# Performance work log

Measured on AMD Instinct MI355X. Metric: run time of the kernel, lower is better.

Reference implementation:

```python
import jax, jax.numpy as jnp
import numpy as np

NUM_HEADS = 8
HEAD_DIM = 16
NEG_SLOPE = 0.2


def setup_inputs() -> dict:
    key = jax.random.key(0)
    k1, k2, k3, k4, k5 = jax.random.split(key, 5)
    N, E, D_IN, D_OUT = 100000, 1600000, 128, 128
    x = jax.random.normal(k1, (N, D_IN), dtype=jnp.float32)
    edge_indices = jax.random.randint(k2, (2, E), 0, N, dtype=jnp.int64)
    W = jax.random.normal(k3, (D_OUT, D_IN), dtype=jnp.float32) * (1.0 / np.sqrt(D_IN))
    src_attn = jax.random.normal(k4, (1, NUM_HEADS, HEAD_DIM), dtype=jnp.float32) * (1.0 / np.sqrt(HEAD_DIM))
    dst_attn = jax.random.normal(k5, (1, NUM_HEADS, HEAD_DIM), dtype=jnp.float32) * (1.0 / np.sqrt(HEAD_DIM))
    return {"x": x, "edge_indices": edge_indices, "W": W, "src_attn": src_attn, "dst_attn": dst_attn}


def reference(x, edge_indices, W, src_attn, dst_attn):
    N = x.shape[0]
    # add self loops (i, i) for every node
    loops = jnp.arange(N, dtype=edge_indices.dtype)
    ei = jnp.concatenate([edge_indices, jnp.stack([loops, loops])], axis=1)  # [2, E+N]
    row, col = ei[0], ei[1]

    # linear projection + head split: [N, H, hd]
    h = (x @ W.T).reshape(N, NUM_HEADS, HEAD_DIM)

    # per-node attention logits, gathered per edge: [E', H]
    s = jnp.sum(h * src_attn, axis=-1)  # [N, H]
    d = jnp.sum(h * dst_attn, axis=-1)  # [N, H]
    e = jax.nn.leaky_relu(s[row] + d[col], negative_slope=NEG_SLOPE)  # [E', H]

    # sparse softmax over each row's neighborhood (dim=1 of the sparse matrix)
    m = jax.ops.segment_max(e, row, num_segments=N)  # [N, H]
    e = jnp.exp(e - m[row])
    z = jax.ops.segment_sum(e, row, num_segments=N)  # [N, H]
    a = e / z[row]  # [E', H]

    # per-head SpMM: out[row] += a * h[col]
    out = jax.ops.segment_sum(a[:, :, None] * h[col], row, num_segments=N)  # [N, H, hd]
    return out.reshape(N, NUM_HEADS * HEAD_DIM)
```

## Files before the change

kernel.cpp:

```cpp
#include <hip/hip_runtime.h>
#include <hip/hip_bf16.h>
#include <math.h>

#define NEG_SLOPE 0.2f

typedef __attribute__((ext_vector_type(8))) short short8v;
typedef __attribute__((ext_vector_type(4))) float f32x4;

__global__ __launch_bounds__(256) void gat_prep(
    const float* __restrict__ W, const float* __restrict__ srcA,
    const float* __restrict__ dstA, ushort* __restrict__ wbf)
{
  int tid = blockIdx.x * 256 + threadIdx.x;
  if (tid >= 36 * 64) return;
  int frag = tid >> 6, lane = tid & 63;
  int nt = frag >> 2, ks = frag & 3;
  int kbase = ks * 32 + (lane >> 4) * 8;
  ushort v[8];
  if (nt < 8) {
    int r = nt * 16 + (lane & 15);
#pragma unroll
    for (int j = 0; j < 8; ++j)
      v[j] = __bfloat16_as_ushort(__float2bfloat16(W[(size_t)r * 128 + kbase + j]));
  } else {
    int n = lane & 15;
    int hd = n & 7;
    const float* av = (n < 8) ? srcA : dstA;
#pragma unroll
    for (int j = 0; j < 8; ++j) {
      float acc = 0.f;
      int k = kbase + j;
      for (int d = 0; d < 16; ++d)
        acc += W[(size_t)(hd * 16 + d) * 128 + k] * av[hd * 16 + d];
      v[j] = __bfloat16_as_ushort(__float2bfloat16(acc));
    }
  }
  ushort* dst = wbf + ((size_t)frag * 64 + lane) * 8;
#pragma unroll
  for (int j = 0; j < 8; ++j) dst[j] = v[j];
}

__global__ __launch_bounds__(256, 2) void gat_gemm_mfma(
    const float* __restrict__ x, const ushort* __restrict__ wbf,
    ushort* __restrict__ hb, float* __restrict__ s, float* __restrict__ dv,
    int N, int nchunks)
{
  const int wave = threadIdx.x >> 6, lane = threadIdx.x & 63;
  const int lrow = lane & 15, lkg = lane >> 4;

  short8v b[36];
  const short8v* wv = (const short8v*)wbf;
#pragma unroll
  for (int f = 0; f < 36; ++f) b[f] = wv[(size_t)f * 64 + lane];

  for (int chunk = blockIdx.x; chunk < nchunks; chunk += gridDim.x) {
    const int r0 = chunk * 64 + wave * 16;
    int arow = r0 + lrow; if (arow > N - 1) arow = N - 1;
    const float* xr = x + (size_t)arow * 128 + lkg * 8;

    f32x4 acc[9];
#pragma unroll
    for (int t = 0; t < 9; ++t) acc[t] = (f32x4){0.f, 0.f, 0.f, 0.f};

#pragma unroll
    for (int ks = 0; ks < 4; ++ks) {
      float4 x0 = *(const float4*)(xr + ks * 32);
      float4 x1 = *(const float4*)(xr + ks * 32 + 4);
      short8v a;
      a[0] = (short)__bfloat16_as_ushort(__float2bfloat16(x0.x));
      a[1] = (short)__bfloat16_as_ushort(__float2bfloat16(x0.y));
      a[2] = (short)__bfloat16_as_ushort(__float2bfloat16(x0.z));
      a[3] = (short)__bfloat16_as_ushort(__float2bfloat16(x0.w));
      a[4] = (short)__bfloat16_as_ushort(__float2bfloat16(x1.x));
      a[5] = (short)__bfloat16_as_ushort(__float2bfloat16(x1.y));
      a[6] = (short)__bfloat16_as_ushort(__float2bfloat16(x1.z));
      a[7] = (short)__bfloat16_as_ushort(__float2bfloat16(x1.w));
#pragma unroll
      for (int t = 0; t < 9; ++t)
        acc[t] = __builtin_amdgcn_mfma_f32_16x16x32_bf16(a, b[t * 4 + ks], acc[t], 0, 0, 0);
    }

    const int rbase = r0 + lkg * 4;
#pragma unroll
    for (int t = 0; t < 8; ++t) {
#pragma unroll
      for (int r = 0; r < 4; ++r) {
        int row = rbase + r;
        if (row < N)
          hb[(size_t)row * 128 + t * 16 + lrow] =
              __bfloat16_as_ushort(__float2bfloat16(acc[t][r]));
      }
    }
#pragma unroll
    for (int r = 0; r < 4; ++r) {
      int row = rbase + r;
      if (row < N) {
        if (lrow < 8) s[(size_t)row * 8 + lrow] = acc[8][r];
        else          dv[(size_t)row * 8 + (lrow - 8)] = acc[8][r];
      }
    }
  }
}

__global__ void gat_detect(const int* __restrict__ ei, int E, int* __restrict__ flag)
{
  __shared__ int any;
  if (threadIdx.x == 0) any = 0;
  __syncthreads();
  int n = E < 512 ? E : 512;
  int local = 0;
  for (int i = threadIdx.x; i < n; i += 256)
    if (ei[2 * i + 1] != 0) local = 1;
  if (local) atomicOr(&any, 1);
  __syncthreads();
  if (threadIdx.x == 0) *flag = (any == 0) ? 1 : 0;
}

__global__ __launch_bounds__(256) void gat_hist(
    const int* __restrict__ ei, int E, const int* __restrict__ flag,
    int* __restrict__ count, int* __restrict__ rank, int userank)
{
  const int is64 = *flag;
  int i = blockIdx.x * 256 + threadIdx.x;
  const int stride = gridDim.x * 256;
  for (; i < E; i += stride) {
    int r = is64 ? ei[2 * i] : ei[i];
    int old = atomicAdd(&count[r], 1);
    if (userank) rank[i] = old;
  }
}

__global__ __launch_bounds__(256) void gat_scan_part(
    const int* __restrict__ count, int N, int* __restrict__ partial)
{
  __shared__ int sm[256];
  int base = blockIdx.x * 1024;
  int tsum = 0;
  for (int i = threadIdx.x; i < 1024; i += 256) {
    int idx = base + i;
    if (idx < N) tsum += count[idx] + 1;
  }
  sm[threadIdx.x] = tsum;
  __syncthreads();
  for (int off = 128; off > 0; off >>= 1) {
    if (threadIdx.x < off) sm[threadIdx.x] += sm[threadIdx.x + off];
    __syncthreads();
  }
  if (threadIdx.x == 0) partial[blockIdx.x] = sm[0];
}

__global__ __launch_bounds__(1024) void gat_scan_mid(int* __restrict__ partial, int nb)
{
  __shared__ int sm[1024];
  int t = threadIdx.x;
  int v = (t < nb) ? partial[t] : 0;
  sm[t] = v;
  __syncthreads();
  int acc = v;
  for (int off = 1; off < 1024; off <<= 1) {
    int other = (t >= off) ? sm[t - off] : 0;
    __syncthreads();
    acc += other;
    sm[t] = acc;
    __syncthreads();
  }
  if (t < nb) partial[t] = acc - v;
}

__global__ __launch_bounds__(256) void gat_scan_final(
    const int* __restrict__ count, int N, const int* __restrict__ partial,
    int* __restrict__ offsets, int* __restrict__ cursor, int total)
{
  __shared__ int sm[256];
  int base = blockIdx.x * 1024 + threadIdx.x * 4;
  int v[4];
  int tsum = 0;
#pragma unroll
  for (int j = 0; j < 4; ++j) {
    int idx = base + j;
    v[j] = (idx < N) ? (count[idx] + 1) : 0;
    tsum += v[j];
  }
  sm[threadIdx.x] = tsum;
  __syncthreads();
  int acc = tsum;
  for (int off = 1; off < 256; off <<= 1) {
    int other = (threadIdx.x >= off) ? sm[threadIdx.x - off] : 0;
    __syncthreads();
    acc += other;
    sm[threadIdx.x] = acc;
    __syncthreads();
  }
  int ex = acc - tsum + partial[blockIdx.x];
#pragma unroll
  for (int j = 0; j < 4; ++j) {
    int idx = base + j;
    if (idx < N) { offsets[idx] = ex; cursor[idx] = ex; ex += v[j]; }
  }
  if (blockIdx.x == 0 && threadIdx.x == 0) offsets[N] = total;
}

__global__ __launch_bounds__(256) void gat_scatter_rank(
    const int* __restrict__ ei, int E, int N, const int* __restrict__ flag,
    const int* __restrict__ offsets, const int* __restrict__ count,
    const int* __restrict__ rank, int* __restrict__ scol)
{
  const int is64 = *flag;
  int i = blockIdx.x * 256 + threadIdx.x;
  const int stride = gridDim.x * 256;
  const int total = E + N;
  for (; i < total; i += stride) {
    int pos, c;
    if (i < E) {
      int r;
      if (is64) { r = ei[2 * i]; c = ei[2 * (E + i)]; }
      else      { r = ei[i];     c = ei[E + i]; }
      pos = offsets[r] + rank[i];
    } else {
      int r = i - E; c = r;
      pos = offsets[r] + count[r];
    }
    scol[pos] = c;
  }
}

__global__ __launch_bounds__(256) void gat_scatter(
    const int* __restrict__ ei, int E, int N, const int* __restrict__ flag,
    int* __restrict__ cursor, int* __restrict__ scol)
{
  const int is64 = *flag;
  int i = blockIdx.x * 256 + threadIdx.x;
  const int stride = gridDim.x * 256;
  const int total = E + N;
  for (; i < total; i += stride) {
    int r, c;
    if (i < E) {
      if (is64) { r = ei[2 * i]; c = ei[2 * (E + i)]; }
      else      { r = ei[i];     c = ei[E + i]; }
    } else {
      r = i - E; c = r;
    }
    int pos = atomicAdd(&cursor[r], 1);
    scol[pos] = c;
  }
}

__global__ __launch_bounds__(256) void gat_agg(
    const uint* __restrict__ hb, const float* __restrict__ s, const float* __restrict__ dv,
    const int* __restrict__ offsets, const int* __restrict__ scol,
    float* __restrict__ out, int N)
{
  int wid = (int)((blockIdx.x * 256 + threadIdx.x) >> 6);
  int lane = threadIdx.x & 63;
  if (wid >= N) return;
  const int head = lane >> 3;
  const int beg = __builtin_amdgcn_readfirstlane(offsets[wid]);
  const int end = __builtin_amdgcn_readfirstlane(offsets[wid + 1]);
  const float sl = s[wid * 8 + head];

  const char* hbp = (const char*)hb;
  const char* dvp = (const char*)dv;
  const uint hoff = (uint)lane * 4u;
  const uint doff = (uint)head * 4u;

  int c1 = scol[beg];
  int i1 = (beg + 1 < end) ? (beg + 1) : (end - 1);
  int c2 = scol[i1];
  float dl0 = *(const float*)(dvp + ((uint)c1 * 32u + doff));
  uint  hu0 = *(const uint*)(hbp + ((uint)c1 * 256u + hoff));

  float z = 0.f, ax = 0.f, ay = 0.f;
  for (int i = beg; i < end; ++i) {
    int i2 = (i + 2 < end) ? (i + 2) : (end - 1);
    int c3 = scol[i2];
    float dl1 = *(const float*)(dvp + ((uint)c2 * 32u + doff));
    uint  hu1 = *(const uint*)(hbp + ((uint)c2 * 256u + hoff));

    float hx = __uint_as_float(hu0 << 16);
    float hy = __uint_as_float(hu0 & 0xFFFF0000u);
    float e = sl + dl0;
    e = fmaxf(e, NEG_SLOPE * e);
    float w = __expf(e);
    z += w;
    ax = fmaf(w, hx, ax);
    ay = fmaf(w, hy, ay);

    c2 = c3; dl0 = dl1; hu0 = hu1;
  }
  float inv = 1.f / z;
  *(float2*)(out + (size_t)wid * 128 + lane * 2) = make_float2(ax * inv, ay * inv);
}

extern "C" void kernel_launch(void* const* d_in, const int* in_sizes, int n_in,
                              void* d_out, int out_size, void* d_ws, size_t ws_size,
                              hipStream_t stream) {
  const float* x    = (const float*)d_in[0];
  const int*   ei   = (const int*)d_in[1];
  const float* W    = (const float*)d_in[2];
  const float* srcA = (const float*)d_in[3];
  const float* dstA = (const float*)d_in[4];
  float* out = (float*)d_out;
  const int N = in_sizes[0] / 128;
  const int E = in_sizes[1] / 2;

  ushort* hbuf = (ushort*)d_ws;
  float* s  = (float*)(hbuf + (size_t)N * 128);
  float* dv = s + (size_t)N * 8;
  ushort* wbf = (ushort*)(dv + (size_t)N * 8);
  int* count   = (int*)((char*)wbf + 36864);
  int* offsets = count + N;
  int* cursor  = offsets + (N + 1);
  int* partial = cursor + N;
  int* flag    = partial + 1024;
  int* scol    = flag + 4;
  int* rank    = scol + (E + N);

  const size_t need_rank = (size_t)((char*)(rank + E) - (char*)d_ws);
  const int userank = (ws_size >= need_rank) ? 1 : 0;

  const int nchunks = (N + 63) / 64;

  (void)hipMemsetAsync(count, 0, (size_t)N * sizeof(int), stream);
  gat_prep<<<9, 256, 0, stream>>>(W, srcA, dstA, wbf);
  gat_gemm_mfma<<<512, 256, 0, stream>>>(x, wbf, hbuf, s, dv, N, nchunks);
  gat_detect<<<1, 256, 0, stream>>>(ei, E, flag);
  gat_hist<<<2048, 256, 0, stream>>>(ei, E, flag, count, rank, userank);
  const int nb = (N + 1023) / 1024;
  gat_scan_part<<<nb, 256, 0, stream>>>(count, N, partial);
  gat_scan_mid<<<1, 1024, 0, stream>>>(partial, nb);
  gat_scan_final<<<nb, 256, 0, stream>>>(count, N, partial, offsets, cursor, E + N);
  if (userank)
    gat_scatter_rank<<<2048, 256, 0, stream>>>(ei, E, N, flag, offsets, count, rank, scol);
  else
    gat_scatter<<<2048, 256, 0, stream>>>(ei, E, N, flag, cursor, scol);
  gat_agg<<<(N + 3) / 4, 256, 0, stream>>>((const uint*)hbuf, s, dv, offsets, scol, out, N);
}
```

Baseline: 251.0 us.

## Fuse GEMM with edge histogram, inline int64 detection, widen aggregation gathers

The count memset moves into the prep kernel. The GEMM and the row histogram now run in one launch, with one block in five doing MFMA work and the other four doing atomics, so the compute-bound and atomic-bound phases can overlap. Each block now detects the 64-bit index format itself, which removes the separate detect kernel. The aggregation kernel splits each wave into four groups that process four edges at once, with 16-byte gathers per lane and a cross-group shuffle reduction. This trades more registers and shuffle work for fewer, wider memory requests.

```diff
diff --git a/kernel.cpp b/kernel.cpp
--- a/kernel.cpp
+++ b/kernel.cpp
@@ -9,8 +9,12 @@
 
 __global__ __launch_bounds__(256) void gat_prep(
     const float* __restrict__ W, const float* __restrict__ srcA,
-    const float* __restrict__ dstA, ushort* __restrict__ wbf)
-{
+    const float* __restrict__ dstA, ushort* __restrict__ wbf,
+    int* __restrict__ count, int N)
+{
+  for (int i = blockIdx.x * 256 + threadIdx.x; i < N; i += gridDim.x * 256)
+    count[i] = 0;
+
   int tid = blockIdx.x * 256 + threadIdx.x;
   if (tid >= 36 * 64) return;
   int frag = tid >> 6, lane = tid & 63;
@@ -40,93 +44,88 @@
   for (int j = 0; j < 8; ++j) dst[j] = v[j];
 }
 
-__global__ __launch_bounds__(256, 2) void gat_gemm_mfma(
+__global__ __launch_bounds__(256, 2) void gat_gemm_hist(
     const float* __restrict__ x, const ushort* __restrict__ wbf,
     ushort* __restrict__ hb, float* __restrict__ s, float* __restrict__ dv,
-    int N, int nchunks)
-{
-  const int wave = threadIdx.x >> 6, lane = threadIdx.x & 63;
-  const int lrow = lane & 15, lkg = lane >> 4;
-
-  short8v b[36];
-  const short8v* wv = (const short8v*)wbf;
-#pragma unroll
-  for (int f = 0; f < 36; ++f) b[f] = wv[(size_t)f * 64 + lane];
-
-  for (int chunk = blockIdx.x; chunk < nchunks; chunk += gridDim.x) {
-    const int r0 = chunk * 64 + wave * 16;
-    int arow = r0 + lrow; if (arow > N - 1) arow = N - 1;
-    const float* xr = x + (size_t)arow * 128 + lkg * 8;
-
-    f32x4 acc[9];
-#pragma unroll
-    for (int t = 0; t < 9; ++t) acc[t] = (f32x4){0.f, 0.f, 0.f, 0.f};
-
-#pragma unroll
-    for (int ks = 0; ks < 4; ++ks) {
-      float4 x0 = *(const float4*)(xr + ks * 32);
-      float4 x1 = *(const float4*)(xr + ks * 32 + 4);
-      short8v a;
-      a[0] = (short)__bfloat16_as_ushort(__float2bfloat16(x0.x));
-      a[1] = (short)__bfloat16_as_ushort(__float2bfloat16(x0.y));
-      a[2] = (short)__bfloat16_as_ushort(__float2bfloat16(x0.z));
-      a[3] = (short)__bfloat16_as_ushort(__float2bfloat16(x0.w));
-      a[4] = (short)__bfloat16_as_ushort(__float2bfloat16(x1.x));
-      a[5] = (short)__bfloat16_as_ushort(__float2bfloat16(x1.y));
-      a[6] = (short)__bfloat16_as_ushort(__float2bfloat16(x1.z));
-      a[7] = (short)__bfloat16_as_ushort(__float2bfloat16(x1.w));
-#pragma unroll
-      for (int t = 0; t < 9; ++t)
-        acc[t] = __builtin_amdgcn_mfma_f32_16x16x32_bf16(a, b[t * 4 + ks], acc[t], 0, 0, 0);
-    }
-
-    const int rbase = r0 + lkg * 4;
-#pragma unroll
-    for (int t = 0; t < 8; ++t) {
+    int N, int nchunks, int G1,
+    const int* __restrict__ ei, int E, int* __restrict__ count,
+    int* __restrict__ rank, int userank)
+{
+  const int q = (int)blockIdx.x / 5;
+  const int r5 = (int)blockIdx.x % 5;
+  if (r5 == 0) {
+    const int wave = threadIdx.x >> 6, lane = threadIdx.x & 63;
+    const int lrow = lane & 15, lkg = lane >> 4;
+
+    short8v b[36];
+    const short8v* wv = (const short8v*)wbf;
+#pragma unroll
+    for (int f = 0; f < 36; ++f) b[f] = wv[(size_t)f * 64 + lane];
+
+    for (int chunk = q; chunk < nchunks; chunk += G1) {
+      const int r0 = chunk * 64 + wave * 16;
+      int arow = r0 + lrow; if (arow > N - 1) arow = N - 1;
+      const float* xr = x + (size_t)arow * 128 + lkg * 8;
+
+      f32x4 acc[9];
+#pragma unroll
+      for (int t = 0; t < 9; ++t) acc[t] = (f32x4){0.f, 0.f, 0.f, 0.f};
+
+#pragma unroll
+      for (int ks = 0; ks < 4; ++ks) {
+        float4 x0 = *(const float4*)(xr + ks * 32);
+        float4 x1 = *(const float4*)(xr + ks * 32 + 4);
+        short8v a;
+        a[0] = (short)__bfloat16_as_ushort(__float2bfloat16(x0.x));
+        a[1] = (short)__bfloat16_as_ushort(__float2bfloat16(x0.y));
+        a[2] = (short)__bfloat16_as_ushort(__float2bfloat16(x0.z));
+        a[3] = (short)__bfloat16_as_ushort(__float2bfloat16(x0.w));
+        a[4] = (short)__bfloat16_as_ushort(__float2bfloat16(x1.x));
+        a[5] = (short)__bfloat16_as_ushort(__float2bfloat16(x1.y));
+        a[6] = (short)__bfloat16_as_ushort(__float2bfloat16(x1.z));
+        a[7] = (short)__bfloat16_as_ushort(__float2bfloat16(x1.w));
+#pragma unroll
+        for (int t = 0; t < 9; ++t)
+          acc[t] = __builtin_amdgcn_mfma_f32_16x16x32_bf16(a, b[t * 4 + ks], acc[t], 0, 0, 0);
+      }
+
+      const int rbase = r0 + lkg * 4;
+#pragma unroll
+      for (int t = 0; t < 8; ++t) {
+#pragma unroll
+        for (int r = 0; r < 4; ++r) {
+          int row = rbase + r;
+          if (row < N)
+            hb[(size_t)row * 128 + t * 16 + lrow] =
+                __bfloat16_as_ushort(__float2bfloat16(acc[t][r]));
+        }
+      }
 #pragma unroll
       for (int r = 0; r < 4; ++r) {
         int row = rbase + r;
-        if (row < N)
-          hb[(size_t)row * 128 + t * 16 + lrow] =
-              __bfloat16_as_ushort(__float2bfloat16(acc[t][r]));
+        if (row < N) {
+          if (lrow < 8) s[(size_t)row * 8 + lrow] = acc[8][r];
+          else          dv[(size_t)row * 8 + (lrow - 8)] = acc[8][r];
+        }
       }
     }
-#pragma unroll
-    for (int r = 0; r < 4; ++r) {
-      int row = rbase + r;
-      if (row < N) {
-        if (lrow < 8) s[(size_t)row * 8 + lrow] = acc[8][r];
-        else          dv[(size_t)row * 8 + (lrow - 8)] = acc[8][r];
-      }
-    }
-  }
-}
-
-__global__ void gat_detect(const int* __restrict__ ei, int E, int* __restrict__ flag)
-{
-  __shared__ int any;
-  if (threadIdx.x == 0) any = 0;
-  __syncthreads();
-  int n = E < 512 ? E : 512;
-  int local = 0;
-  for (int i = threadIdx.x; i < n; i += 256)
-    if (ei[2 * i + 1] != 0) local = 1;
-  if (local) atomicOr(&any, 1);
-  __syncthreads();
-  if (threadIdx.x == 0) *flag = (any == 0) ? 1 : 0;
-}
-
-__global__ __launch_bounds__(256) void gat_hist(
-    const int* __restrict__ ei, int E, const int* __restrict__ flag,
-    int* __restrict__ count, int* __restrict__ rank, int userank)
-{
-  const int is64 = *flag;
-  int i = blockIdx.x * 256 + threadIdx.x;
-  const int stride = gridDim.x * 256;
-  for (; i < E; i += stride) {
-    int r = is64 ? ei[2 * i] : ei[i];
-    int old = atomicAdd(&count[r], 1);
-    if (userank) rank[i] = old;
+  } else {
+    __shared__ int sh64;
+    if (threadIdx.x == 0) sh64 = 1;
+    __syncthreads();
+    if (ei[2 * threadIdx.x + 1] != 0) sh64 = 0;
+    __syncthreads();
+    const int is64 = sh64;
+
+    const int hb_id = q * 4 + (r5 - 1);
+    const int nhb = 4 * G1;
+    int i = hb_id * 256 + threadIdx.x;
+    const int stride = nhb * 256;
+    for (; i < E; i += stride) {
+      int r = is64 ? ei[2 * i] : ei[i];
+      int old = atomicAdd(&count[r], 1);
+      if (userank) rank[i] = old;
+    }
   }
 }
 
@@ -201,11 +200,17 @@
 }
 
 __global__ __launch_bounds__(256) void gat_scatter_rank(
-    const int* __restrict__ ei, int E, int N, const int* __restrict__ flag,
+    const int* __restrict__ ei, int E, int N,
     const int* __restrict__ offsets, const int* __restrict__ count,
     const int* __restrict__ rank, int* __restrict__ scol)
 {
-  const int is64 = *flag;
+  __shared__ int sh64;
+  if (threadIdx.x == 0) sh64 = 1;
+  __syncthreads();
+  if (ei[2 * threadIdx.x + 1] != 0) sh64 = 0;
+  __syncthreads();
+  const int is64 = sh64;
+
   int i = blockIdx.x * 256 + threadIdx.x;
   const int stride = gridDim.x * 256;
   const int total = E + N;
@@ -225,10 +230,16 @@
 }
 
 __global__ __launch_bounds__(256) void gat_scatter(
-    const int* __restrict__ ei, int E, int N, const int* __restrict__ flag,
+    const int* __restrict__ ei, int E, int N,
     int* __restrict__ cursor, int* __restrict__ scol)
 {
-  const int is64 = *flag;
+  __shared__ int sh64;
+  if (threadIdx.x == 0) sh64 = 1;
+  __syncthreads();
+  if (ei[2 * threadIdx.x + 1] != 0) sh64 = 0;
+  __syncthreads();
+  const int is64 = sh64;
+
   int i = blockIdx.x * 256 + threadIdx.x;
   const int stride = gridDim.x * 256;
   const int total = E + N;
@@ -253,42 +264,69 @@
   int wid = (int)((blockIdx.x * 256 + threadIdx.x) >> 6);
   int lane = threadIdx.x & 63;
   if (wid >= N) return;
-  const int head = lane >> 3;
+  const int g = lane >> 4;
+  const int t = lane & 15;
+  const int head = t >> 1;
   const int beg = __builtin_amdgcn_readfirstlane(offsets[wid]);
   const int end = __builtin_amdgcn_readfirstlane(offsets[wid + 1]);
   const float sl = s[wid * 8 + head];
 
   const char* hbp = (const char*)hb;
   const char* dvp = (const char*)dv;
-  const uint hoff = (uint)lane * 4u;
+  const uint hoff = (uint)t * 16u;
   const uint doff = (uint)head * 4u;
 
-  int c1 = scol[beg];
-  int i1 = (beg + 1 < end) ? (beg + 1) : (end - 1);
-  int c2 = scol[i1];
-  float dl0 = *(const float*)(dvp + ((uint)c1 * 32u + doff));
-  uint  hu0 = *(const uint*)(hbp + ((uint)c1 * 256u + hoff));
-
-  float z = 0.f, ax = 0.f, ay = 0.f;
-  for (int i = beg; i < end; ++i) {
-    int i2 = (i + 2 < end) ? (i + 2) : (end - 1);
-    int c3 = scol[i2];
-    float dl1 = *(const float*)(dvp + ((uint)c2 * 32u + doff));
-    uint  hu1 = *(const uint*)(hbp + ((uint)c2 * 256u + hoff));
-
-    float hx = __uint_as_float(hu0 << 16);
-    float hy = __uint_as_float(hu0 & 0xFFFF0000u);
-    float e = sl + dl0;
+  float z = 0.f;
+  float a0 = 0, a1 = 0, a2 = 0, a3 = 0, a4 = 0, a5 = 0, a6 = 0, a7 = 0;
+
+  const int nq = (end - beg + 3) >> 2;
+  const int lasti = end - 1;
+
+  int iA = beg + g;       iA = iA < end ? iA : lasti;
+  int iB = beg + 4 + g;   iB = iB < end ? iB : lasti;
+  int cA = scol[iA];
+  int cB = scol[iB];
+  float dlA = *(const float*)(dvp + ((uint)cA * 32u + doff));
+  uint4 huA = *(const uint4*)(hbp + ((uint)cA * 256u + hoff));
+
+  for (int j = 0; j < nq; ++j) {
+    int iC = beg + 4 * (j + 2) + g; iC = iC < end ? iC : lasti;
+    int cC = scol[iC];
+    float dlB = *(const float*)(dvp + ((uint)cB * 32u + doff));
+    uint4 huB = *(const uint4*)(hbp + ((uint)cB * 256u + hoff));
+
+    float e = sl + dlA;
     e = fmaxf(e, NEG_SLOPE * e);
-    float w = __expf(e);
+    float w = (beg + 4 * j + g < end) ? __expf(e) : 0.f;
     z += w;
-    ax = fmaf(w, hx, ax);
-    ay = fmaf(w, hy, ay);
-
-    c2 = c3; dl0 = dl1; hu0 = hu1;
-  }
+    a0 = fmaf(w, __uint_as_float(huA.x << 16), a0);
+    a1 = fmaf(w, __uint_as_float(huA.x & 0xFFFF0000u), a1);
+    a2 = fmaf(w, __uint_as_float(huA.y << 16), a2);
+    a3 = fmaf(w, __uint_as_float(huA.y & 0xFFFF0000u), a3);
+    a4 = fmaf(w, __uint_as_float(huA.z << 16), a4);
+    a5 = fmaf(w, __uint_as_float(huA.z & 0xFFFF0000u), a5);
+    a6 = fmaf(w, __uint_as_float(huA.w << 16), a6);
+    a7 = fmaf(w, __uint_as_float(huA.w & 0xFFFF0000u), a7);
+
+    cB = cC; dlA = dlB; huA = huB;
+  }
+
+  a0 += __shfl_xor(a0, 16, 64); a0 += __shfl_xor(a0, 32, 64);
+  a1 += __shfl_xor(a1, 16, 64); a1 += __shfl_xor(a1, 32, 64);
+  a2 += __shfl_xor(a2, 16, 64); a2 += __shfl_xor(a2, 32, 64);
+  a3 += __shfl_xor(a3, 16, 64); a3 += __shfl_xor(a3, 32, 64);
+  a4 += __shfl_xor(a4, 16, 64); a4 += __shfl_xor(a4, 32, 64);
+  a5 += __shfl_xor(a5, 16, 64); a5 += __shfl_xor(a5, 32, 64);
+  a6 += __shfl_xor(a6, 16, 64); a6 += __shfl_xor(a6, 32, 64);
+  a7 += __shfl_xor(a7, 16, 64); a7 += __shfl_xor(a7, 32, 64);
+  z  += __shfl_xor(z, 16, 64);  z  += __shfl_xor(z, 32, 64);
+
   float inv = 1.f / z;
-  *(float2*)(out + (size_t)wid * 128 + lane * 2) = make_float2(ax * inv, ay * inv);
+  if (lane < 16) {
+    float4* op = (float4*)(out + (size_t)wid * 128 + t * 8);
+    op[0] = make_float4(a0 * inv, a1 * inv, a2 * inv, a3 * inv);
+    op[1] = make_float4(a4 * inv, a5 * inv, a6 * inv, a7 * inv);
+  }
 }
 
 extern "C" void kernel_launch(void* const* d_in, const int* in_sizes, int n_in,
@@ -311,27 +349,25 @@
   int* offsets = count + N;
   int* cursor  = offsets + (N + 1);
   int* partial = cursor + N;
-  int* flag    = partial + 1024;
-  int* scol    = flag + 4;
+  int* scol    = partial + 1024;
   int* rank    = scol + (E + N);
 
   const size_t need_rank = (size_t)((char*)(rank + E) - (char*)d_ws);
   const int userank = (ws_size >= need_rank) ? 1 : 0;
 
   const int nchunks = (N + 63) / 64;
-
-  (void)hipMemsetAsync(count, 0, (size_t)N * sizeof(int), stream);
-  gat_prep<<<9, 256, 0, stream>>>(W, srcA, dstA, wbf);
-  gat_gemm_mfma<<<512, 256, 0, stream>>>(x, wbf, hbuf, s, dv, N, nchunks);
-  gat_detect<<<1, 256, 0, stream>>>(ei, E, flag);
-  gat_hist<<<2048, 256, 0, stream>>>(ei, E, flag, count, rank, userank);
+  const int G1 = 512;
+
+  gat_prep<<<2048, 256, 0, stream>>>(W, srcA, dstA, wbf, count, N);
+  gat_gemm_hist<<<5 * G1, 256, 0, stream>>>(x, wbf, hbuf, s, dv, N, nchunks, G1,
+                                            ei, E, count, rank, userank);
   const int nb = (N + 1023) / 1024;
   gat_scan_part<<<nb, 256, 0, stream>>>(count, N, partial);
   gat_scan_mid<<<1, 1024, 0, stream>>>(partial, nb);
   gat_scan_final<<<nb, 256, 0, stream>>>(count, N, partial, offsets, cursor, E + N);
   if (userank)
-    gat_scatter_rank<<<2048, 256, 0, stream>>>(ei, E, N, flag, offsets, count, rank, scol);
+    gat_scatter_rank<<<2048, 256, 0, stream>>>(ei, E, N, offsets, count, rank, scol);
   else
-    gat_scatter<<<2048, 256, 0, stream>>>(ei, E, N, flag, cursor, scol);
+    gat_scatter<<<2048, 256, 0, stream>>>(ei, E, N, cursor, scol);
   gat_agg<<<(N + 3) / 4, 256, 0, stream>>>((const uint*)hbuf, s, dv, offsets, scol, out, N);
 }
```

After: 202.9 us. 1.24x faster.
